# Kernel optimization log

Measured on AMD Instinct MI355X. Metric: run time of the kernel, lower is better.

## Reference

```python
import jax, jax.numpy as jnp
import numpy as np

BITS = 4
GROUP = 128
IN_F = 4096
OUT_F = 4096
MAXQ = (1 << BITS) - 1  # 15
PACK = 32 // BITS       # 8 values per int32


def setup_inputs() -> dict:
    key = jax.random.key(0)
    k1, k2, k3, k4, k5 = jax.random.split(key, 5)
    x = jax.random.normal(k1, (4, 2048, IN_F), dtype=jnp.float32)
    qweight = jax.random.randint(k2, (IN_F // 32 * BITS, OUT_F), 0, 2147483647, dtype=jnp.int32)
    qzeros = jax.random.randint(k3, (IN_F // GROUP, OUT_F // 32 * BITS), 0, 2147483647, dtype=jnp.int32)
    scales = jax.random.uniform(k4, (IN_F // GROUP, OUT_F), dtype=jnp.float32, minval=0.001, maxval=0.01)
    bias = jax.random.normal(k5, (OUT_F,), dtype=jnp.float32) * 0.01
    return {"x": x, "qweight": qweight, "qzeros": qzeros, "scales": scales, "bias": bias}


def _dequant(qweight, qzeros, scales):
    shifts = jnp.arange(0, 32, BITS, dtype=jnp.int32)  # [PACK]
    # zeros: [n_groups, out//PACK, PACK] -> [n_groups, 1, OUT_F]; +1 per GPTQ convention
    zeros = ((qzeros[:, :, None] >> shifts[None, None, :]) & MAXQ) + 1
    zeros = zeros.reshape(-1, 1, OUT_F).astype(scales.dtype)
    # weight: [rows, PACK, OUT_F] -> [n_groups, GROUP, OUT_F]
    w = (qweight[:, None, :] >> shifts[None, :, None]) & MAXQ
    w = w.reshape(-1, GROUP, OUT_F).astype(scales.dtype)
    W = scales[:, None, :] * (w - zeros)
    return W.reshape(IN_F, OUT_F)


def reference(x, qweight, qzeros, scales, bias):
    W = _dequant(qweight, qzeros, scales)          # [IN_F, OUT_F]
    out_shape = x.shape[:-1] + (OUT_F,)
    out = x.reshape(-1, IN_F) @ W                  # [B*S, OUT_F]
    out = out + bias
    return out.reshape(out_shape)
```

## Files before the change

kernel.cpp:

```cpp
#include <hip/hip_runtime.h>
#include <hip/hip_bf16.h>

#define IN_F 4096
#define OUT_F 4096
#define M_ROWS 8192
#define GROUP 128

#define KT_TILES (IN_F / 32)


typedef __attribute__((ext_vector_type(8))) short short8;
typedef __attribute__((ext_vector_type(4))) float floatx4;

__device__ __forceinline__ unsigned short f2bf(float f) {
    unsigned int u = __builtin_bit_cast(unsigned int, f);
    u += 0x7fffu + ((u >> 16) & 1u);
    return (unsigned short)(u >> 16);
}

__device__ __forceinline__ void load_lds16(const unsigned short* g, unsigned short* l) {
    __builtin_amdgcn_global_load_lds(
        (const __attribute__((address_space(1))) void*)g,
        (__attribute__((address_space(3))) void*)l,
        16, 0, 0);
}

__global__ __launch_bounds__(256) void convert_x_kernel(const float* __restrict__ x,
                                                        unsigned short* __restrict__ xb) {
    __shared__ unsigned short tile[16 * 256];

    const int t  = threadIdx.x;
    const int m0 = blockIdx.y * 16;
    const int k0 = blockIdx.x * 256;

    {
        const int r = t & 15;
        const int c = t >> 4;
        const float4* src = (const float4*)(x + (size_t)(m0 + r) * IN_F + k0 + c * 16);
        float4 f[4];
#pragma unroll
        for (int i = 0; i < 4; ++i) f[i] = src[i];
        const float* fs = (const float*)f;
#pragma unroll
        for (int h = 0; h < 2; ++h) {
            const int kl = c * 16 + h * 8;
            const int kt_l = kl >> 5;
            const int q    = (kl >> 3) & 3;
            union { unsigned short us[8]; uint4 v; } o;
#pragma unroll
            for (int j = 0; j < 8; ++j) o.us[j] = f2bf(fs[h * 8 + j]);
            *(uint4*)&tile[kt_l * 512 + (q * 16 + (t & 15)) * 8] = o.v;
        }
    }

    __syncthreads();

    {
        unsigned short* dst = xb + ((size_t)blockIdx.y * KT_TILES + blockIdx.x * 8) * 512;
        *(uint4*)&dst[t * 8]        = *(const uint4*)&tile[t * 8];
        *(uint4*)&dst[2048 + t * 8] = *(const uint4*)&tile[2048 + t * 8];
    }
}

#define DQ_KP 32
#define DQ_N  64

__global__ __launch_bounds__(256) void dequant_kernel(const int* __restrict__ qw,
                                                      const int* __restrict__ qz,
                                                      const float* __restrict__ sc,
                                                      unsigned short* __restrict__ wt) {
    __shared__ unsigned short tile[4 * 8 * 512];

    const int t   = threadIdx.x;
    const int kp0 = blockIdx.x * DQ_KP;
    const int n0  = blockIdx.y * DQ_N;

    {
        const int kp_l = t >> 3;
        const int nq   = t & 7;
        const int kp   = kp0 + kp_l;
        const int g    = kp >> 4;
        const int nb   = n0 + nq * 8;

        const uint4 q0 = *(const uint4*)&qw[(size_t)kp * OUT_F + nb];
        const uint4 q1 = *(const uint4*)&qw[(size_t)kp * OUT_F + nb + 4];
        const unsigned zq = (unsigned)qz[g * (OUT_F / 8) + (nb >> 3)];
        const float4 s0 = *(const float4*)&sc[(size_t)g * OUT_F + nb];
        const float4 s1 = *(const float4*)&sc[(size_t)g * OUT_F + nb + 4];

        unsigned qv[8] = {q0.x, q0.y, q0.z, q0.w, q1.x, q1.y, q1.z, q1.w};
        float    sv[8] = {s0.x, s0.y, s0.z, s0.w, s1.x, s1.y, s1.z, s1.w};

        const int kt_l  = kp_l >> 2;
        const int q_out = kp_l & 3;
        const int tn_l  = nq >> 1;

#pragma unroll
        for (int c = 0; c < 8; ++c) {
            const unsigned q = qv[c];
            const float zero = (float)(((zq >> (4 * c)) & 15u) + 1u);
            const float s = sv[c];
            const int r = (nq * 8 + c) & 15;
            union { unsigned short us[8]; uint4 v; } o;
#pragma unroll
            for (int j = 0; j < 8; ++j) {
                const float w = (float)((q >> (4 * j)) & 15u);
                o.us[j] = f2bf(s * (w - zero));
            }
            *(uint4*)&tile[(tn_l * 8 + kt_l) * 512 + (q_out * 16 + r) * 8] = o.v;
        }
    }

    __syncthreads();

    {
        const int tn0 = blockIdx.y * 4;
        const int kt0 = blockIdx.x * 8;
#pragma unroll
        for (int tn_l = 0; tn_l < 4; ++tn_l) {
            unsigned short* dst = wt + ((size_t)(tn0 + tn_l) * KT_TILES + kt0) * 512;
            const unsigned short* srcl = &tile[tn_l * 4096];
            *(uint4*)&dst[t * 8]        = *(const uint4*)&srcl[t * 8];
            *(uint4*)&dst[2048 + t * 8] = *(const uint4*)&srcl[2048 + t * 8];
        }
    }
}

__global__ __launch_bounds__(512, 2) void gemm_kernel(const unsigned short* __restrict__ xb,
                                                      const unsigned short* __restrict__ wt,
                                                      const float* __restrict__ bias,
                                                      float* __restrict__ out) {
    __shared__ unsigned short As[3 * 16 * 512];
    __shared__ unsigned short Bs[3 * 16 * 512];

    const int tid  = threadIdx.x;
    const int wid  = tid >> 6;
    const int lane = tid & 63;

    const int bid = blockIdx.x;
    const int swz = (bid & 7) * 64 + (bid >> 3);
    const int bx  = swz & 15;
    const int by  = swz >> 4;

    const int wm = wid & 1;
    const int wn = wid >> 1;

    const int TM0 = by * 16;
    const int TN0 = bx * 16;

    floatx4 acc[8][4] = {};

    const unsigned short* gA0 = xb + ((size_t)(TM0 + wid)     * KT_TILES) * 512 + lane * 8;
    const unsigned short* gA1 = xb + ((size_t)(TM0 + 8 + wid) * KT_TILES) * 512 + lane * 8;
    const unsigned short* gB0 = wt + ((size_t)(TN0 + wid)     * KT_TILES) * 512 + lane * 8;
    const unsigned short* gB1 = wt + ((size_t)(TN0 + 8 + wid) * KT_TILES) * 512 + lane * 8;

    unsigned short* lA0 = &As[wid * 512];
    unsigned short* lA1 = &As[(8 + wid) * 512];
    unsigned short* lB0 = &Bs[wid * 512];
    unsigned short* lB1 = &Bs[(8 + wid) * 512];

    const unsigned short* aBase = &As[(wm * 8) * 512 + lane * 8];
    const unsigned short* bBase = &Bs[(wn * 4) * 512 + lane * 8];

#define STAGE_A(buf, s) do { \
        load_lds16(gA0 + (size_t)(s) * 512, lA0 + (buf) * 8192); \
        load_lds16(gA1 + (size_t)(s) * 512, lA1 + (buf) * 8192); } while (0)
#define STAGE_B(buf, s) do { \
        load_lds16(gB0 + (size_t)(s) * 512, lB0 + (buf) * 8192); \
        load_lds16(gB1 + (size_t)(s) * 512, lB1 + (buf) * 8192); } while (0)

    STAGE_A(0, 0); STAGE_B(0, 0);
    STAGE_A(1, 1); STAGE_B(1, 1);
    asm volatile("s_waitcnt vmcnt(4)" ::: "memory");
    asm volatile("s_barrier" ::: "memory");

    int cur = 0, pre = 2;
#pragma unroll 1
    for (int t = 0; t < 128; ++t) {
        const unsigned short* ab = aBase + cur * 8192;
        const unsigned short* bb = bBase + cur * 8192;

        short8 a[4], b[4];

#pragma unroll
        for (int j = 0; j < 4; ++j) b[j] = *(const short8*)(bb + j * 512);
#pragma unroll
        for (int i = 0; i < 4; ++i) a[i] = *(const short8*)(ab + i * 512);
        if (t < 126) { STAGE_A(pre, t + 2); }
        asm volatile("s_barrier" ::: "memory");
        asm volatile("s_waitcnt lgkmcnt(0)" ::: "memory");
        __builtin_amdgcn_sched_barrier(0);
        __builtin_amdgcn_s_setprio(1);
#pragma unroll
        for (int i = 0; i < 4; ++i)
#pragma unroll
            for (int j = 0; j < 4; ++j)
                acc[i][j] = __builtin_amdgcn_mfma_f32_16x16x32_bf16(a[i], b[j], acc[i][j], 0, 0, 0);
        __builtin_amdgcn_s_setprio(0);
        __builtin_amdgcn_sched_barrier(0);
        asm volatile("s_barrier" ::: "memory");

#pragma unroll
        for (int i = 0; i < 4; ++i) a[i] = *(const short8*)(ab + (4 + i) * 512);
        if (t < 126) {
            STAGE_B(pre, t + 2);
            asm volatile("s_waitcnt vmcnt(4)" ::: "memory");
        } else if (t == 126) {
            asm volatile("s_waitcnt vmcnt(0)" ::: "memory");
        }
        asm volatile("s_barrier" ::: "memory");
        asm volatile("s_waitcnt lgkmcnt(0)" ::: "memory");
        __builtin_amdgcn_sched_barrier(0);
        __builtin_amdgcn_s_setprio(1);
#pragma unroll
        for (int i = 0; i < 4; ++i)
#pragma unroll
            for (int j = 0; j < 4; ++j)
                acc[4 + i][j] = __builtin_amdgcn_mfma_f32_16x16x32_bf16(a[i], b[j], acc[4 + i][j], 0, 0, 0);
        __builtin_amdgcn_s_setprio(0);
        __builtin_amdgcn_sched_barrier(0);
        asm volatile("s_barrier" ::: "memory");

        cur = (cur == 2) ? 0 : cur + 1;
        pre = (pre == 2) ? 0 : pre + 1;
    }
#undef STAGE_A
#undef STAGE_B

    const int mrow = TM0 * 16 + wm * 128 + (lane >> 4) * 4;
    const int ncol = TN0 * 16 + wn * 64 + (lane & 15);
#pragma unroll
    for (int j = 0; j < 4; ++j) {
        const int n = ncol + j * 16;
        const float bv = bias[n];
#pragma unroll
        for (int i = 0; i < 8; ++i) {
            const int m = mrow + i * 16;
#pragma unroll
            for (int r = 0; r < 4; ++r)
                out[(size_t)(m + r) * OUT_F + n] = acc[i][j][r] + bv;
        }
    }
}

extern "C" void kernel_launch(void* const* d_in, const int* in_sizes, int n_in,
                              void* d_out, int out_size, void* d_ws, size_t ws_size,
                              hipStream_t stream) {
    const float* x    = (const float*)d_in[0];
    const int*   qw   = (const int*)d_in[1];
    const int*   qz   = (const int*)d_in[2];
    const float* sc   = (const float*)d_in[3];
    const float* bias = (const float*)d_in[4];
    float* out = (float*)d_out;

    unsigned short* xb = (unsigned short*)d_ws;
    unsigned short* wt = xb + (size_t)M_ROWS * IN_F;

    convert_x_kernel<<<dim3(IN_F / 256, M_ROWS / 16), 256, 0, stream>>>(x, xb);
    dequant_kernel<<<dim3(IN_F / 8 / DQ_KP, OUT_F / DQ_N), 256, 0, stream>>>(qw, qz, sc, wt);
    gemm_kernel<<<dim3((M_ROWS / 256) * (OUT_F / 256)), 512, 0, stream>>>(xb, wt, bias, out);
}
```

Before: 490.6 us.

## Fuse int4 weight dequantization into GEMM main loop, drop separate dequant kernel

Removes the standalone dequant kernel and its bf16 weight buffer. The GEMM now loads packed int4 weights, scales and zeros from global memory into registers two k-steps ahead, then dequantizes and writes bf16 into a double-buffered LDS tile between MFMA phases. This saves one launch and the round-trip of a bf16 weight matrix through HBM. In exchange every block repeats the dequant ALU work (32 row-blocks recompute the same weights), uses more registers, and takes on a more complex wait/barrier schedule.

```diff
diff --git a/kernel.cpp b/kernel.cpp
--- a/kernel.cpp
+++ b/kernel.cpp
@@ -25,6 +25,16 @@
         16, 0, 0);
 }
 
+__device__ __forceinline__ uint4 dq8(unsigned q, float s, float zero) {
+    union { unsigned short us[8]; uint4 v; } o;
+#pragma unroll
+    for (int j = 0; j < 8; ++j) {
+        const float w = (float)((q >> (4 * j)) & 15u);
+        o.us[j] = f2bf(s * (w - zero));
+    }
+    return o.v;
+}
+
 __global__ __launch_bounds__(256) void convert_x_kernel(const float* __restrict__ x,
                                                         unsigned short* __restrict__ xb) {
     __shared__ unsigned short tile[16 * 256];
@@ -62,76 +72,14 @@
     }
 }
 
-#define DQ_KP 32
-#define DQ_N  64
-
-__global__ __launch_bounds__(256) void dequant_kernel(const int* __restrict__ qw,
+__global__ __launch_bounds__(512, 2) void gemm_kernel(const unsigned short* __restrict__ xb,
+                                                      const int* __restrict__ qw,
                                                       const int* __restrict__ qz,
                                                       const float* __restrict__ sc,
-                                                      unsigned short* __restrict__ wt) {
-    __shared__ unsigned short tile[4 * 8 * 512];
-
-    const int t   = threadIdx.x;
-    const int kp0 = blockIdx.x * DQ_KP;
-    const int n0  = blockIdx.y * DQ_N;
-
-    {
-        const int kp_l = t >> 3;
-        const int nq   = t & 7;
-        const int kp   = kp0 + kp_l;
-        const int g    = kp >> 4;
-        const int nb   = n0 + nq * 8;
-
-        const uint4 q0 = *(const uint4*)&qw[(size_t)kp * OUT_F + nb];
-        const uint4 q1 = *(const uint4*)&qw[(size_t)kp * OUT_F + nb + 4];
-        const unsigned zq = (unsigned)qz[g * (OUT_F / 8) + (nb >> 3)];
-        const float4 s0 = *(const float4*)&sc[(size_t)g * OUT_F + nb];
-        const float4 s1 = *(const float4*)&sc[(size_t)g * OUT_F + nb + 4];
-
-        unsigned qv[8] = {q0.x, q0.y, q0.z, q0.w, q1.x, q1.y, q1.z, q1.w};
-        float    sv[8] = {s0.x, s0.y, s0.z, s0.w, s1.x, s1.y, s1.z, s1.w};
-
-        const int kt_l  = kp_l >> 2;
-        const int q_out = kp_l & 3;
-        const int tn_l  = nq >> 1;
-
-#pragma unroll
-        for (int c = 0; c < 8; ++c) {
-            const unsigned q = qv[c];
-            const float zero = (float)(((zq >> (4 * c)) & 15u) + 1u);
-            const float s = sv[c];
-            const int r = (nq * 8 + c) & 15;
-            union { unsigned short us[8]; uint4 v; } o;
-#pragma unroll
-            for (int j = 0; j < 8; ++j) {
-                const float w = (float)((q >> (4 * j)) & 15u);
-                o.us[j] = f2bf(s * (w - zero));
-            }
-            *(uint4*)&tile[(tn_l * 8 + kt_l) * 512 + (q_out * 16 + r) * 8] = o.v;
-        }
-    }
-
-    __syncthreads();
-
-    {
-        const int tn0 = blockIdx.y * 4;
-        const int kt0 = blockIdx.x * 8;
-#pragma unroll
-        for (int tn_l = 0; tn_l < 4; ++tn_l) {
-            unsigned short* dst = wt + ((size_t)(tn0 + tn_l) * KT_TILES + kt0) * 512;
-            const unsigned short* srcl = &tile[tn_l * 4096];
-            *(uint4*)&dst[t * 8]        = *(const uint4*)&srcl[t * 8];
-            *(uint4*)&dst[2048 + t * 8] = *(const uint4*)&srcl[2048 + t * 8];
-        }
-    }
-}
-
-__global__ __launch_bounds__(512, 2) void gemm_kernel(const unsigned short* __restrict__ xb,
-                                                      const unsigned short* __restrict__ wt,
                                                       const float* __restrict__ bias,
                                                       float* __restrict__ out) {
-    __shared__ unsigned short As[3 * 16 * 512];
-    __shared__ unsigned short Bs[3 * 16 * 512];
+    __shared__ unsigned short As[3 * 8192];
+    __shared__ unsigned short Bs[2 * 8192];
 
     const int tid  = threadIdx.x;
     const int wid  = tid >> 6;
@@ -146,90 +94,118 @@
     const int wn = wid >> 1;
 
     const int TM0 = by * 16;
-    const int TN0 = bx * 16;
+    const int n0  = bx * 256;
 
     floatx4 acc[8][4] = {};
 
     const unsigned short* gA0 = xb + ((size_t)(TM0 + wid)     * KT_TILES) * 512 + lane * 8;
     const unsigned short* gA1 = xb + ((size_t)(TM0 + 8 + wid) * KT_TILES) * 512 + lane * 8;
-    const unsigned short* gB0 = wt + ((size_t)(TN0 + wid)     * KT_TILES) * 512 + lane * 8;
-    const unsigned short* gB1 = wt + ((size_t)(TN0 + 8 + wid) * KT_TILES) * 512 + lane * 8;
-
     unsigned short* lA0 = &As[wid * 512];
     unsigned short* lA1 = &As[(8 + wid) * 512];
-    unsigned short* lB0 = &Bs[wid * 512];
-    unsigned short* lB1 = &Bs[(8 + wid) * 512];
+
+    const int cq  = (tid >> 4) & 3;
+    const int cr  = tid & 15;
+    const int nt1 = tid >> 6;
+    const int nB1 = n0 + nt1 * 16 + cr;
+    const int nB2 = nB1 + 128;
+    const int c0  = 4 * (nB1 & 7);
 
     const unsigned short* aBase = &As[(wm * 8) * 512 + lane * 8];
     const unsigned short* bBase = &Bs[(wn * 4) * 512 + lane * 8];
+    unsigned short* lBw = &Bs[tid * 8];
 
 #define STAGE_A(buf, s) do { \
         load_lds16(gA0 + (size_t)(s) * 512, lA0 + (buf) * 8192); \
         load_lds16(gA1 + (size_t)(s) * 512, lA1 + (buf) * 8192); } while (0)
-#define STAGE_B(buf, s) do { \
-        load_lds16(gB0 + (size_t)(s) * 512, lB0 + (buf) * 8192); \
-        load_lds16(gB1 + (size_t)(s) * 512, lB1 + (buf) * 8192); } while (0)
-
-    STAGE_A(0, 0); STAGE_B(0, 0);
-    STAGE_A(1, 1); STAGE_B(1, 1);
-    asm volatile("s_waitcnt vmcnt(4)" ::: "memory");
+
+#define LOAD_B(P, s) do { \
+        const int kp_ = (s) * 4 + cq; const int g_ = (s) >> 2; \
+        P##_q1 = (unsigned)qw[(size_t)kp_ * OUT_F + nB1]; \
+        P##_q2 = (unsigned)qw[(size_t)kp_ * OUT_F + nB2]; \
+        P##_s1 = sc[(size_t)g_ * OUT_F + nB1]; \
+        P##_s2 = sc[(size_t)g_ * OUT_F + nB2]; \
+        P##_z1 = (unsigned)qz[g_ * (OUT_F / 8) + (nB1 >> 3)]; \
+        P##_z2 = (unsigned)qz[g_ * (OUT_F / 8) + (nB2 >> 3)]; } while (0)
+
+#define DQ_WRITE(P, wb) do { \
+        const float z1_ = (float)(((P##_z1 >> c0) & 15u) + 1u); \
+        const float z2_ = (float)(((P##_z2 >> c0) & 15u) + 1u); \
+        *(uint4*)(lBw + (wb) * 8192)        = dq8(P##_q1, P##_s1, z1_); \
+        *(uint4*)(lBw + (wb) * 8192 + 4096) = dq8(P##_q2, P##_s2, z2_); } while (0)
+
+    unsigned s0_q1, s0_q2, s0_z1, s0_z2, s1_q1, s1_q2, s1_z1, s1_z2;
+    float    s0_s1, s0_s2, s1_s1, s1_s2;
+    unsigned p_q1, p_q2, p_z1, p_z2;
+    float    p_s1, p_s2;
+
+    LOAD_B(p, 0);
+    LOAD_B(s1, 1);
+    STAGE_A(0, 0);
+    STAGE_A(1, 1);
+    DQ_WRITE(p, 0);
+    asm volatile("s_waitcnt vmcnt(0)" ::: "memory");
+    asm volatile("s_waitcnt lgkmcnt(0)" ::: "memory");
+    __builtin_amdgcn_sched_barrier(0);
     asm volatile("s_barrier" ::: "memory");
 
     int cur = 0, pre = 2;
+
+#define KSTEP(T, BCUR, L, U)  \
+  { \
+    const unsigned short* ab = aBase + cur * 8192; \
+    const unsigned short* bb = bBase + (BCUR) * 8192; \
+    short8 a[4], b[4]; \
+    _Pragma("unroll") for (int j = 0; j < 4; ++j) b[j] = *(const short8*)(bb + j * 512); \
+    _Pragma("unroll") for (int i = 0; i < 4; ++i) a[i] = *(const short8*)(ab + i * 512); \
+    if ((T) < 126) { \
+      STAGE_A(pre, (T) + 2); \
+      LOAD_B(L, (T) + 2); \
+    } \
+    asm volatile("s_barrier" ::: "memory"); \
+    asm volatile("s_waitcnt lgkmcnt(0)" ::: "memory"); \
+    __builtin_amdgcn_sched_barrier(0); \
+    __builtin_amdgcn_s_setprio(1); \
+    _Pragma("unroll") for (int i = 0; i < 4; ++i) \
+      _Pragma("unroll") for (int j = 0; j < 4; ++j) \
+        acc[i][j] = __builtin_amdgcn_mfma_f32_16x16x32_bf16(a[i], b[j], acc[i][j], 0, 0, 0); \
+    __builtin_amdgcn_s_setprio(0); \
+    __builtin_amdgcn_sched_barrier(0); \
+    asm volatile("s_barrier" ::: "memory"); \
+     \
+    _Pragma("unroll") for (int i = 0; i < 4; ++i) a[i] = *(const short8*)(ab + (4 + i) * 512); \
+    if ((T) < 126) { asm volatile("s_waitcnt vmcnt(8)" ::: "memory"); } \
+    else if ((T) == 126) { asm volatile("s_waitcnt vmcnt(0)" ::: "memory"); } \
+    asm volatile("s_barrier" ::: "memory"); \
+    asm volatile("s_waitcnt lgkmcnt(0)" ::: "memory"); \
+    __builtin_amdgcn_sched_barrier(0); \
+    __builtin_amdgcn_s_setprio(1); \
+    _Pragma("unroll") for (int i = 0; i < 4; ++i) \
+      _Pragma("unroll") for (int j = 0; j < 4; ++j) \
+        acc[4 + i][j] = __builtin_amdgcn_mfma_f32_16x16x32_bf16(a[i], b[j], acc[4 + i][j], 0, 0, 0); \
+    if ((T) < 127) { \
+      DQ_WRITE(U, (BCUR) ^ 1); \
+    } \
+    __builtin_amdgcn_s_setprio(0); \
+    __builtin_amdgcn_sched_barrier(0); \
+    asm volatile("s_waitcnt lgkmcnt(0)" ::: "memory"); \
+    asm volatile("s_barrier" ::: "memory"); \
+    cur = (cur == 2) ? 0 : cur + 1; \
+    pre = (pre == 2) ? 0 : pre + 1; \
+  }
+
 #pragma unroll 1
-    for (int t = 0; t < 128; ++t) {
-        const unsigned short* ab = aBase + cur * 8192;
-        const unsigned short* bb = bBase + cur * 8192;
-
-        short8 a[4], b[4];
-
-#pragma unroll
-        for (int j = 0; j < 4; ++j) b[j] = *(const short8*)(bb + j * 512);
-#pragma unroll
-        for (int i = 0; i < 4; ++i) a[i] = *(const short8*)(ab + i * 512);
-        if (t < 126) { STAGE_A(pre, t + 2); }
-        asm volatile("s_barrier" ::: "memory");
-        asm volatile("s_waitcnt lgkmcnt(0)" ::: "memory");
-        __builtin_amdgcn_sched_barrier(0);
-        __builtin_amdgcn_s_setprio(1);
-#pragma unroll
-        for (int i = 0; i < 4; ++i)
-#pragma unroll
-            for (int j = 0; j < 4; ++j)
-                acc[i][j] = __builtin_amdgcn_mfma_f32_16x16x32_bf16(a[i], b[j], acc[i][j], 0, 0, 0);
-        __builtin_amdgcn_s_setprio(0);
-        __builtin_amdgcn_sched_barrier(0);
-        asm volatile("s_barrier" ::: "memory");
-
-#pragma unroll
-        for (int i = 0; i < 4; ++i) a[i] = *(const short8*)(ab + (4 + i) * 512);
-        if (t < 126) {
-            STAGE_B(pre, t + 2);
-            asm volatile("s_waitcnt vmcnt(4)" ::: "memory");
-        } else if (t == 126) {
-            asm volatile("s_waitcnt vmcnt(0)" ::: "memory");
-        }
-        asm volatile("s_barrier" ::: "memory");
-        asm volatile("s_waitcnt lgkmcnt(0)" ::: "memory");
-        __builtin_amdgcn_sched_barrier(0);
-        __builtin_amdgcn_s_setprio(1);
-#pragma unroll
-        for (int i = 0; i < 4; ++i)
-#pragma unroll
-            for (int j = 0; j < 4; ++j)
-                acc[4 + i][j] = __builtin_amdgcn_mfma_f32_16x16x32_bf16(a[i], b[j], acc[4 + i][j], 0, 0, 0);
-        __builtin_amdgcn_s_setprio(0);
-        __builtin_amdgcn_sched_barrier(0);
-        asm volatile("s_barrier" ::: "memory");
-
-        cur = (cur == 2) ? 0 : cur + 1;
-        pre = (pre == 2) ? 0 : pre + 1;
-    }
+    for (int i = 0; i < 64; ++i) {
+        const int t0 = i * 2;
+        KSTEP(t0,     0, s0, s1);
+        KSTEP(t0 + 1, 1, s1, s0);
+    }
+#undef KSTEP
 #undef STAGE_A
-#undef STAGE_B
+#undef LOAD_B
+#undef DQ_WRITE
 
     const int mrow = TM0 * 16 + wm * 128 + (lane >> 4) * 4;
-    const int ncol = TN0 * 16 + wn * 64 + (lane & 15);
+    const int ncol = n0 + wn * 64 + (lane & 15);
 #pragma unroll
     for (int j = 0; j < 4; ++j) {
         const int n = ncol + j * 16;
@@ -255,9 +231,7 @@
     float* out = (float*)d_out;
 
     unsigned short* xb = (unsigned short*)d_ws;
-    unsigned short* wt = xb + (size_t)M_ROWS * IN_F;
 
     convert_x_kernel<<<dim3(IN_F / 256, M_ROWS / 16), 256, 0, stream>>>(x, xb);
-    dequant_kernel<<<dim3(IN_F / 8 / DQ_KP, OUT_F / DQ_N), 256, 0, stream>>>(qw, qz, sc, wt);
-    gemm_kernel<<<dim3((M_ROWS / 256) * (OUT_F / 256)), 512, 0, stream>>>(xb, wt, bias, out);
-}
+    gemm_kernel<<<dim3((M_ROWS / 256) * (OUT_F / 256)), 512, 0, stream>>>(xb, qw, qz, sc, bias, out);
+}
```

Result: slower. 592.9 us (+20.9%).

## Deepen GEMM LDS pipeline to four stages with one barrier per k-step

Applied to the files above, without the earlier changes.

The GEMM main loop moves from a 3-buffer ring to a 4-buffer ring in LDS, prefetching three k-tiles ahead, and issues all A and B global-to-LDS loads together. It also drops three of the four s_barriers per iteration down to one, overlapping the second half of the A-fragment LDS reads with the first MFMA block via split lgkmcnt waits. LDS use rises to 128 KB per block, which may limit occupancy to one block per CU despite launch_bounds(512,2). The x-conversion kernel also swaps its row/column thread mapping so that adjacent threads read contiguous memory.

```diff
diff --git a/kernel.cpp b/kernel.cpp
--- a/kernel.cpp
+++ b/kernel.cpp
@@ -34,8 +34,8 @@
     const int k0 = blockIdx.x * 256;
 
     {
-        const int r = t & 15;
-        const int c = t >> 4;
+        const int r = t >> 4;
+        const int c = t & 15;
         const float4* src = (const float4*)(x + (size_t)(m0 + r) * IN_F + k0 + c * 16);
         float4 f[4];
 #pragma unroll
@@ -49,7 +49,7 @@
             union { unsigned short us[8]; uint4 v; } o;
 #pragma unroll
             for (int j = 0; j < 8; ++j) o.us[j] = f2bf(fs[h * 8 + j]);
-            *(uint4*)&tile[kt_l * 512 + (q * 16 + (t & 15)) * 8] = o.v;
+            *(uint4*)&tile[kt_l * 512 + (q * 16 + r) * 8] = o.v;
         }
     }
 
@@ -130,8 +130,8 @@
                                                       const unsigned short* __restrict__ wt,
                                                       const float* __restrict__ bias,
                                                       float* __restrict__ out) {
-    __shared__ unsigned short As[3 * 16 * 512];
-    __shared__ unsigned short Bs[3 * 16 * 512];
+    __shared__ unsigned short As[4 * 8192];
+    __shared__ unsigned short Bs[4 * 8192];
 
     const int tid  = threadIdx.x;
     const int wid  = tid >> 6;
@@ -163,33 +163,36 @@
     const unsigned short* aBase = &As[(wm * 8) * 512 + lane * 8];
     const unsigned short* bBase = &Bs[(wn * 4) * 512 + lane * 8];
 
-#define STAGE_A(buf, s) do { \
+#define STAGE_AB(buf, s) do { \
         load_lds16(gA0 + (size_t)(s) * 512, lA0 + (buf) * 8192); \
-        load_lds16(gA1 + (size_t)(s) * 512, lA1 + (buf) * 8192); } while (0)
-#define STAGE_B(buf, s) do { \
+        load_lds16(gA1 + (size_t)(s) * 512, lA1 + (buf) * 8192); \
         load_lds16(gB0 + (size_t)(s) * 512, lB0 + (buf) * 8192); \
         load_lds16(gB1 + (size_t)(s) * 512, lB1 + (buf) * 8192); } while (0)
 
-    STAGE_A(0, 0); STAGE_B(0, 0);
-    STAGE_A(1, 1); STAGE_B(1, 1);
-    asm volatile("s_waitcnt vmcnt(4)" ::: "memory");
+    STAGE_AB(0, 0);
+    STAGE_AB(1, 1);
+    STAGE_AB(2, 2);
+    asm volatile("s_waitcnt vmcnt(8)" ::: "memory");
     asm volatile("s_barrier" ::: "memory");
 
-    int cur = 0, pre = 2;
 #pragma unroll 1
     for (int t = 0; t < 128; ++t) {
+        const int cur = t & 3;
         const unsigned short* ab = aBase + cur * 8192;
         const unsigned short* bb = bBase + cur * 8192;
 
-        short8 a[4], b[4];
-
+        short8 a[8], b[4];
 #pragma unroll
         for (int j = 0; j < 4; ++j) b[j] = *(const short8*)(bb + j * 512);
 #pragma unroll
         for (int i = 0; i < 4; ++i) a[i] = *(const short8*)(ab + i * 512);
-        if (t < 126) { STAGE_A(pre, t + 2); }
-        asm volatile("s_barrier" ::: "memory");
-        asm volatile("s_waitcnt lgkmcnt(0)" ::: "memory");
+        if (t < 125) STAGE_AB((t + 3) & 3, t + 3);
+        __builtin_amdgcn_sched_barrier(0);
+#pragma unroll
+        for (int i = 4; i < 8; ++i) a[i] = *(const short8*)(ab + i * 512);
+        __builtin_amdgcn_sched_barrier(0);
+
+        asm volatile("s_waitcnt lgkmcnt(4)" ::: "memory");
         __builtin_amdgcn_sched_barrier(0);
         __builtin_amdgcn_s_setprio(1);
 #pragma unroll
@@ -199,34 +202,28 @@
                 acc[i][j] = __builtin_amdgcn_mfma_f32_16x16x32_bf16(a[i], b[j], acc[i][j], 0, 0, 0);
         __builtin_amdgcn_s_setprio(0);
         __builtin_amdgcn_sched_barrier(0);
-        asm volatile("s_barrier" ::: "memory");
-
-#pragma unroll
-        for (int i = 0; i < 4; ++i) a[i] = *(const short8*)(ab + (4 + i) * 512);
-        if (t < 126) {
-            STAGE_B(pre, t + 2);
+
+        asm volatile("s_waitcnt lgkmcnt(0)" ::: "memory");
+        __builtin_amdgcn_sched_barrier(0);
+        __builtin_amdgcn_s_setprio(1);
+#pragma unroll
+        for (int i = 0; i < 4; ++i)
+#pragma unroll
+            for (int j = 0; j < 4; ++j)
+                acc[4 + i][j] = __builtin_amdgcn_mfma_f32_16x16x32_bf16(a[4 + i], b[j], acc[4 + i][j], 0, 0, 0);
+        __builtin_amdgcn_s_setprio(0);
+        __builtin_amdgcn_sched_barrier(0);
+
+        if (t < 125) {
+            asm volatile("s_waitcnt vmcnt(8)" ::: "memory");
+        } else if (t == 125) {
             asm volatile("s_waitcnt vmcnt(4)" ::: "memory");
         } else if (t == 126) {
             asm volatile("s_waitcnt vmcnt(0)" ::: "memory");
         }
-        asm volatile("s_barrier" ::: "memory");
-        asm volatile("s_waitcnt lgkmcnt(0)" ::: "memory");
-        __builtin_amdgcn_sched_barrier(0);
-        __builtin_amdgcn_s_setprio(1);
-#pragma unroll
-        for (int i = 0; i < 4; ++i)
-#pragma unroll
-            for (int j = 0; j < 4; ++j)
-                acc[4 + i][j] = __builtin_amdgcn_mfma_f32_16x16x32_bf16(a[i], b[j], acc[4 + i][j], 0, 0, 0);
-        __builtin_amdgcn_s_setprio(0);
-        __builtin_amdgcn_sched_barrier(0);
-        asm volatile("s_barrier" ::: "memory");
-
-        cur = (cur == 2) ? 0 : cur + 1;
-        pre = (pre == 2) ? 0 : pre + 1;
-    }
-#undef STAGE_A
-#undef STAGE_B
+        if (t < 127) asm volatile("s_barrier" ::: "memory");
+    }
+#undef STAGE_AB
 
     const int mrow = TM0 * 16 + wm * 128 + (lane >> 4) * 4;
     const int ncol = TN0 * 16 + wn * 64 + (lane & 15);
```

New measurement: 512.7 us. +4.5%, slower.
